# Kernel optimization log

Measured on AMD Instinct MI355X. Metric: run time of the kernel, lower is better.

The kernel has to match this reference:

```python
import jax, jax.numpy as jnp
import numpy as np

D_MODEL = 1024
N_HEADS = 16
D_K = D_MODEL // N_HEADS


def setup_inputs() -> dict:
    key = jax.random.key(0)
    k1, k2, k3, k4, k5 = jax.random.split(key, 5)
    scale = 1.0 / np.sqrt(D_MODEL)
    return {
        "x": jax.random.normal(k1, (4, 2048, D_MODEL), dtype=jnp.float32),
        "w_qkv": jax.random.normal(k2, (D_MODEL, 3 * D_MODEL), dtype=jnp.float32) * scale,
        "b_qkv": jnp.zeros((3 * D_MODEL,), dtype=jnp.float32),
        "w_out": jax.random.normal(k3, (D_MODEL, D_MODEL), dtype=jnp.float32) * scale,
        "b_out": jnp.zeros((D_MODEL,), dtype=jnp.float32),
    }


def reference(x, w_qkv, b_qkv, w_out, b_out):
    B, T, E = x.shape
    qkv = x @ w_qkv + b_qkv                      # [B,T,3E]
    qkv = qkv.reshape(B, T, 3, N_HEADS, D_K)
    qkv = jnp.transpose(qkv, (2, 0, 3, 1, 4))    # [3,B,H,T,d_k]
    q, k, v = qkv[0], qkv[1], qkv[2]
    scores = jnp.einsum("bhqd,bhkd->bhqk", q, k) / jnp.sqrt(jnp.float32(D_K))
    attn = jax.nn.softmax(scores, axis=-1)       # [B,H,T,T]
    out = jnp.einsum("bhqk,bhkd->bhqd", attn, v)  # [B,H,T,d_k]
    out = jnp.transpose(out, (0, 2, 1, 3)).reshape(B, T, E)
    return out @ w_out + b_out
```

## Files before the change

kernel.cpp:

```cpp
#include <hip/hip_runtime.h>
#include <hip/hip_bf16.h>

typedef __attribute__((ext_vector_type(8))) short short8;
typedef __attribute__((ext_vector_type(4))) float f32x4;
typedef __attribute__((ext_vector_type(4))) unsigned short ushort4v;
typedef unsigned short ushort;

#define DEVI static __device__ __forceinline__

DEVI ushort f2bf(float f){
  union { float f; unsigned u; } v; v.f = f;
  unsigned r = v.u + 0x7fffu + ((v.u >> 16) & 1u);
  return (ushort)(r >> 16);
}
DEVI float bf2f(ushort u){
  union { unsigned u; float f; } v; v.u = ((unsigned)u) << 16;
  return v.f;
}

DEVI void gload_lds16(const void* g, void* l){
  __builtin_amdgcn_global_load_lds(
      (const __attribute__((address_space(1))) void*)g,
      (__attribute__((address_space(3))) void*)l, 16, 0, 0);
}

__global__ __launch_bounds__(256) void cast_bf16(const float4* __restrict__ in,
                                                 ushort* __restrict__ out, int n4){
  int i = blockIdx.x * 256 + threadIdx.x;
  if (i < n4){
    float4 v = in[i];
    ushort4v o = { f2bf(v.x), f2bf(v.y), f2bf(v.z), f2bf(v.w) };
    *(ushort4v*)&out[(size_t)i * 4] = o;
  }
}

template<int SPLIT>
__global__ __launch_bounds__(256) void transpose_cast(const float* __restrict__ in,
                                                      ushort* __restrict__ outT,
                                                      ushort* __restrict__ outLo,
                                                      int R, int C){
  __shared__ float tile[64][65];
  const int r0 = blockIdx.y * 64, c0 = blockIdx.x * 64;
  const int t = threadIdx.x;
  for (int it = 0; it < 16; ++it){
    int idx = it * 256 + t; int rr = idx >> 6, cc = idx & 63;
    tile[rr][cc] = in[(size_t)(r0 + rr) * C + (c0 + cc)];
  }
  __syncthreads();
  for (int it = 0; it < 16; ++it){
    int idx = it * 256 + t; int oc = idx >> 6, orow = idx & 63;
    float v = tile[orow][oc];
    ushort hi = f2bf(v);
    size_t o = (size_t)(c0 + oc) * R + (r0 + orow);
    outT[o] = hi;
    if (SPLIT) outLo[o] = f2bf(v - bf2f(hi));
  }
}

__global__ __launch_bounds__(256) void gemm_qk(const ushort* __restrict__ A,
                                               const ushort* __restrict__ BT,
                                               const float* __restrict__ bias,
                                               ushort* __restrict__ Qo,
                                               ushort* __restrict__ Ko){
  constexpr int K = 1024;
  constexpr float QSCALE = 0.18033688011112042f;
  __shared__ __align__(16) ushort As[128 * 32];
  __shared__ __align__(16) ushort Bs[128 * 32];
  const int tid = threadIdx.x, w = tid >> 6, l = tid & 63;
  const int wr = w >> 1, wc = w & 1;
  const int mtile = blockIdx.y * 128, ntile = blockIdx.x * 128;

  f32x4 acc[4][4];
  for (int m = 0; m < 4; ++m) for (int n = 0; n < 4; ++n)
    for (int r = 0; r < 4; ++r) acc[m][n][r] = 0.f;

  const int c0 = 2 * w, c1 = 2 * w + 1;
  const ushort* aG0 = A  + (size_t)(mtile + c0 * 16 + (l >> 2)) * K + (l & 3) * 8;
  const ushort* aG1 = A  + (size_t)(mtile + c1 * 16 + (l >> 2)) * K + (l & 3) * 8;
  const ushort* bG0 = BT + (size_t)(ntile + c0 * 16 + (l >> 2)) * K + (l & 3) * 8;
  const ushort* bG1 = BT + (size_t)(ntile + c1 * 16 + (l >> 2)) * K + (l & 3) * 8;

  for (int kt = 0; kt < K / 32; ++kt){
    __syncthreads();
    gload_lds16(aG0 + kt * 32, &As[c0 * 512]);
    gload_lds16(aG1 + kt * 32, &As[c1 * 512]);
    gload_lds16(bG0 + kt * 32, &Bs[c0 * 512]);
    gload_lds16(bG1 + kt * 32, &Bs[c1 * 512]);
    __syncthreads();
    short8 aF[4], bF[4];
    for (int m = 0; m < 4; ++m)
      aF[m] = *(const short8*)&As[(wr * 64 + m * 16 + (l & 15)) * 32 + (l >> 4) * 8];
    for (int n = 0; n < 4; ++n)
      bF[n] = *(const short8*)&Bs[(wc * 64 + n * 16 + (l & 15)) * 32 + (l >> 4) * 8];
    for (int m = 0; m < 4; ++m)
      for (int n = 0; n < 4; ++n)
        acc[m][n] = __builtin_amdgcn_mfma_f32_16x16x32_bf16(aF[m], bF[n], acc[m][n], 0, 0, 0);
  }

  for (int nf = 0; nf < 4; ++nf){
    int ncol = ntile + wc * 64 + nf * 16 + (l & 15);
    float bv = bias[ncol];
    int isQ = (ncol < 1024) ? 1 : 0;
    int h = (ncol >> 6) & 15, d = ncol & 63;
    ushort* dst = isQ ? Qo : Ko;
    float sc = isQ ? QSCALE : 1.0f;
    for (int m = 0; m < 4; ++m){
      int rbase = mtile + wr * 64 + m * 16 + (l >> 4) * 4;
      for (int r = 0; r < 4; ++r){
        int row = rbase + r;
        int b = row >> 11, t = row & 2047;
        dst[((size_t)(b * 16 + h) * 2048 + t) * 64 + d] = f2bf((acc[m][nf][r] + bv) * sc);
      }
    }
  }
}

__global__ __launch_bounds__(256) void gemm_vT(const ushort* __restrict__ A,
                                               const ushort* __restrict__ BT,
                                               const float* __restrict__ bias,
                                               ushort* __restrict__ VT){
  constexpr int K = 1024;
  __shared__ __align__(16) ushort As[128 * 32];
  __shared__ __align__(16) ushort Bs[128 * 32];
  __shared__ __align__(16) ushort LT[128][136];
  const int tid = threadIdx.x, w = tid >> 6, l = tid & 63;
  const int wr = w >> 1, wc = w & 1;
  const int mtile = blockIdx.y * 128, ntv = blockIdx.x * 128;

  f32x4 acc[4][4];
  for (int m = 0; m < 4; ++m) for (int n = 0; n < 4; ++n)
    for (int r = 0; r < 4; ++r) acc[m][n][r] = 0.f;

  const int c0 = 2 * w, c1 = 2 * w + 1;
  const ushort* aG0 = A  + (size_t)(mtile + c0 * 16 + (l >> 2)) * K + (l & 3) * 8;
  const ushort* aG1 = A  + (size_t)(mtile + c1 * 16 + (l >> 2)) * K + (l & 3) * 8;
  const ushort* bG0 = BT + (size_t)(2048 + ntv + c0 * 16 + (l >> 2)) * K + (l & 3) * 8;
  const ushort* bG1 = BT + (size_t)(2048 + ntv + c1 * 16 + (l >> 2)) * K + (l & 3) * 8;

  for (int kt = 0; kt < K / 32; ++kt){
    __syncthreads();
    gload_lds16(aG0 + kt * 32, &As[c0 * 512]);
    gload_lds16(aG1 + kt * 32, &As[c1 * 512]);
    gload_lds16(bG0 + kt * 32, &Bs[c0 * 512]);
    gload_lds16(bG1 + kt * 32, &Bs[c1 * 512]);
    __syncthreads();
    short8 aF[4], bF[4];
    for (int m = 0; m < 4; ++m)
      aF[m] = *(const short8*)&As[(wr * 64 + m * 16 + (l & 15)) * 32 + (l >> 4) * 8];
    for (int n = 0; n < 4; ++n)
      bF[n] = *(const short8*)&Bs[(wc * 64 + n * 16 + (l & 15)) * 32 + (l >> 4) * 8];
    for (int m = 0; m < 4; ++m)
      for (int n = 0; n < 4; ++n)
        acc[m][n] = __builtin_amdgcn_mfma_f32_16x16x32_bf16(aF[m], bF[n], acc[m][n], 0, 0, 0);
  }

  for (int nf = 0; nf < 4; ++nf){
    int cl = wc * 64 + nf * 16 + (l & 15);
    float bv = bias[2048 + ntv + cl];
    for (int m = 0; m < 4; ++m){
      int rl = wr * 64 + m * 16 + (l >> 4) * 4;
      for (int r = 0; r < 4; ++r)
        LT[cl][rl + r] = f2bf(acc[m][nf][r] + bv);
    }
  }
  __syncthreads();
  const int b = mtile >> 11, t0 = mtile & 2047;
  for (int p = 0; p < 8; ++p){
    int idx = p * 256 + tid;
    int col = idx >> 4, tc = idx & 15;
    int ncol = ntv + col;
    int h = ncol >> 6, d = ncol & 63;
    short8 v = *(const short8*)&LT[col][tc * 8];
    *(short8*)&VT[((size_t)(b * 16 + h) * 64 + d) * 2048 + t0 + tc * 8] = v;
  }
}

__global__ __launch_bounds__(256) void attn_fwd(const ushort* __restrict__ Q,
                                                const ushort* __restrict__ Kb,
                                                const ushort* __restrict__ VT,
                                                ushort* __restrict__ Ohi,
                                                ushort* __restrict__ Olo){
  __shared__ __align__(16) ushort Ks[2][64 * 64];
  __shared__ __align__(16) ushort Vs[2][64 * 64];
  __shared__ __align__(16) ushort Ps[4][16][72];
  const int tid = threadIdx.x, w = tid >> 6, l = tid & 63;
  const int h = l >> 4, q = l & 15;
  const int bh = blockIdx.y, qbase = blockIdx.x * 64;
  const ushort* Qp = Q  + (size_t)bh * 2048 * 64;
  const ushort* Kp = Kb + (size_t)bh * 2048 * 64;
  const ushort* Vp = VT + (size_t)bh * 64 * 2048;

  constexpr float DEFER_THR = 8.0f;

  const int qrow = qbase + w * 16 + q;
  short8 qf0 = *(const short8*)&Qp[(size_t)qrow * 64 + h * 8];
  short8 qf1 = *(const short8*)&Qp[(size_t)qrow * 64 + 32 + h * 8];

  float mrow = -1e30f, lrow = 0.f;
  f32x4 oacc[4];
  for (int c = 0; c < 4; ++c) for (int r = 0; r < 4; ++r) oacc[c][r] = 0.f;

  const int c0 = 2 * w, c1 = 2 * w + 1;
  const int ssrc = ((l & 7) ^ (l >> 3)) * 8;
  const int sr0 = c0 * 8 + (l >> 3), sr1 = c1 * 8 + (l >> 3);
  const int rxor = (q & 7) * 8;

  gload_lds16(Kp + (size_t)sr0 * 64 + ssrc, &Ks[0][c0 * 512]);
  gload_lds16(Kp + (size_t)sr1 * 64 + ssrc, &Ks[0][c1 * 512]);
  gload_lds16(Vp + (size_t)sr0 * 2048 + ssrc, &Vs[0][c0 * 512]);
  gload_lds16(Vp + (size_t)sr1 * 2048 + ssrc, &Vs[0][c1 * 512]);
  __syncthreads();

  int cur = 0;
  for (int kt = 0; kt < 32; ++kt){
    if (kt < 31){
      const int kb = (kt + 1) * 64;
      gload_lds16(Kp + (size_t)(kb + sr0) * 64 + ssrc, &Ks[cur ^ 1][c0 * 512]);
      gload_lds16(Kp + (size_t)(kb + sr1) * 64 + ssrc, &Ks[cur ^ 1][c1 * 512]);
      gload_lds16(Vp + (size_t)sr0 * 2048 + kb + ssrc, &Vs[cur ^ 1][c0 * 512]);
      gload_lds16(Vp + (size_t)sr1 * 2048 + kb + ssrc, &Vs[cur ^ 1][c1 * 512]);
    }
    const ushort* ks = Ks[cur];
    const ushort* vs = Vs[cur];

    f32x4 s[4];
    for (int nf = 0; nf < 4; ++nf) for (int r = 0; r < 4; ++r) s[nf][r] = 0.f;
    __builtin_amdgcn_s_setprio(1);
    for (int nf = 0; nf < 4; ++nf){
      int rb = (nf * 16 + q) * 64;
      short8 kf0 = *(const short8*)&ks[rb + ((h * 8)      ^ rxor)];
      short8 kf1 = *(const short8*)&ks[rb + ((h * 8 + 32) ^ rxor)];
      s[nf] = __builtin_amdgcn_mfma_f32_16x16x32_bf16(kf0, qf0, s[nf], 0, 0, 0);
      s[nf] = __builtin_amdgcn_mfma_f32_16x16x32_bf16(kf1, qf1, s[nf], 0, 0, 0);
    }
    __builtin_amdgcn_s_setprio(0);

    float pm01 = fmaxf(fmaxf(s[0][0], s[0][1]), fmaxf(s[0][2], s[0][3]));
    float pm23 = fmaxf(fmaxf(s[1][0], s[1][1]), fmaxf(s[1][2], s[1][3]));
    float pm45 = fmaxf(fmaxf(s[2][0], s[2][1]), fmaxf(s[2][2], s[2][3]));
    float pm67 = fmaxf(fmaxf(s[3][0], s[3][1]), fmaxf(s[3][2], s[3][3]));
    float pmax = fmaxf(fmaxf(pm01, pm23), fmaxf(pm45, pm67));
    pmax = fmaxf(pmax, __shfl_xor(pmax, 16));
    pmax = fmaxf(pmax, __shfl_xor(pmax, 32));

    if (!__all(pmax <= mrow + DEFER_THR)){
      float mn = fmaxf(mrow, pmax);
      float alpha = __builtin_amdgcn_exp2f(mrow - mn);
      mrow = mn;
      lrow *= alpha;
      for (int c = 0; c < 4; ++c)
        for (int r = 0; r < 4; ++r) oacc[c][r] *= alpha;
    }

    float rsum = 0.f;
    for (int nf = 0; nf < 4; ++nf)
      for (int r = 0; r < 4; ++r){
        float p = __builtin_amdgcn_exp2f(s[nf][r] - mrow);
        s[nf][r] = p; rsum += p;
      }
    rsum += __shfl_xor(rsum, 16);
    rsum += __shfl_xor(rsum, 32);
    lrow += rsum;

    for (int nf = 0; nf < 4; ++nf){
      unsigned pk01, pk23;
      asm("v_cvt_pk_bf16_f32 %0, %1, %2" : "=v"(pk01) : "v"(s[nf][0]), "v"(s[nf][1]));
      asm("v_cvt_pk_bf16_f32 %0, %1, %2" : "=v"(pk23) : "v"(s[nf][2]), "v"(s[nf][3]));
      int key = nf * 16 + 4 * h;
      *(unsigned*)&Ps[w][q][key]     = pk01;
      *(unsigned*)&Ps[w][q][key + 2] = pk23;
    }

    __builtin_amdgcn_s_setprio(1);
    for (int st = 0; st < 2; ++st){
      short8 pf = *(const short8*)&Ps[w][q][st * 32 + h * 8];
      for (int c = 0; c < 4; ++c){
        int vb = (c * 16 + q) * 64;
        short8 vf = *(const short8*)&vs[vb + ((st * 32 + h * 8) ^ rxor)];
        oacc[c] = __builtin_amdgcn_mfma_f32_16x16x32_bf16(vf, pf, oacc[c], 0, 0, 0);
      }
    }
    __builtin_amdgcn_s_setprio(0);

    __syncthreads();
    cur ^= 1;
  }

  const int b = bh >> 4, hh = bh & 15;
  float inv = 1.0f / lrow;
  size_t rowoff = ((size_t)(b * 2048 + qrow)) * 1024 + hh * 64;
  for (int c = 0; c < 4; ++c){
    int d0 = c * 16 + 4 * h;
    for (int pr = 0; pr < 2; ++pr){
      float v0 = oacc[c][2 * pr]     * inv;
      float v1 = oacc[c][2 * pr + 1] * inv;
      ushort h0 = f2bf(v0), h1 = f2bf(v1);
      unsigned hi = (unsigned)h0 | ((unsigned)h1 << 16);
      unsigned lo = (unsigned)f2bf(v0 - bf2f(h0)) | ((unsigned)f2bf(v1 - bf2f(h1)) << 16);
      *(unsigned*)&Ohi[rowoff + d0 + 2 * pr] = hi;
      *(unsigned*)&Olo[rowoff + d0 + 2 * pr] = lo;
    }
  }
}

__global__ __launch_bounds__(256) void gemm_out(const ushort* __restrict__ Ah,
                                                const ushort* __restrict__ Al,
                                                const ushort* __restrict__ BhT,
                                                const ushort* __restrict__ BlT,
                                                const float* __restrict__ bias,
                                                float* __restrict__ out){
  constexpr int K = 1024;
  __shared__ __align__(16) ushort Ash[128 * 32], Asl[128 * 32];
  __shared__ __align__(16) ushort Bsh[128 * 32], Bsl[128 * 32];
  const int tid = threadIdx.x, w = tid >> 6, l = tid & 63;
  const int wr = w >> 1, wc = w & 1;
  const int mtile = blockIdx.y * 128, ntile = blockIdx.x * 128;

  f32x4 acc[4][4];
  for (int m = 0; m < 4; ++m) for (int n = 0; n < 4; ++n)
    for (int r = 0; r < 4; ++r) acc[m][n][r] = 0.f;

  const int c0 = 2 * w, c1 = 2 * w + 1;
  const size_t aOff0 = (size_t)(mtile + c0 * 16 + (l >> 2)) * K + (l & 3) * 8;
  const size_t aOff1 = (size_t)(mtile + c1 * 16 + (l >> 2)) * K + (l & 3) * 8;
  const size_t bOff0 = (size_t)(ntile + c0 * 16 + (l >> 2)) * K + (l & 3) * 8;
  const size_t bOff1 = (size_t)(ntile + c1 * 16 + (l >> 2)) * K + (l & 3) * 8;

  for (int kt = 0; kt < K / 32; ++kt){
    __syncthreads();
    gload_lds16(Ah  + aOff0 + kt * 32, &Ash[c0 * 512]);
    gload_lds16(Ah  + aOff1 + kt * 32, &Ash[c1 * 512]);
    gload_lds16(Al  + aOff0 + kt * 32, &Asl[c0 * 512]);
    gload_lds16(Al  + aOff1 + kt * 32, &Asl[c1 * 512]);
    gload_lds16(BhT + bOff0 + kt * 32, &Bsh[c0 * 512]);
    gload_lds16(BhT + bOff1 + kt * 32, &Bsh[c1 * 512]);
    gload_lds16(BlT + bOff0 + kt * 32, &Bsl[c0 * 512]);
    gload_lds16(BlT + bOff1 + kt * 32, &Bsl[c1 * 512]);
    __syncthreads();
    short8 aH[4], aL[4], bH[4], bL[4];
    for (int m = 0; m < 4; ++m){
      int o = (wr * 64 + m * 16 + (l & 15)) * 32 + (l >> 4) * 8;
      aH[m] = *(const short8*)&Ash[o];
      aL[m] = *(const short8*)&Asl[o];
    }
    for (int n = 0; n < 4; ++n){
      int o = (wc * 64 + n * 16 + (l & 15)) * 32 + (l >> 4) * 8;
      bH[n] = *(const short8*)&Bsh[o];
      bL[n] = *(const short8*)&Bsl[o];
    }
    for (int m = 0; m < 4; ++m)
      for (int n = 0; n < 4; ++n){
        acc[m][n] = __builtin_amdgcn_mfma_f32_16x16x32_bf16(aH[m], bH[n], acc[m][n], 0, 0, 0);
        acc[m][n] = __builtin_amdgcn_mfma_f32_16x16x32_bf16(aH[m], bL[n], acc[m][n], 0, 0, 0);
        acc[m][n] = __builtin_amdgcn_mfma_f32_16x16x32_bf16(aL[m], bH[n], acc[m][n], 0, 0, 0);
      }
  }

  for (int nf = 0; nf < 4; ++nf){
    int ncol = ntile + wc * 64 + nf * 16 + (l & 15);
    float bv = bias[ncol];
    for (int m = 0; m < 4; ++m){
      int rbase = mtile + wr * 64 + m * 16 + (l >> 4) * 4;
      for (int r = 0; r < 4; ++r)
        out[(size_t)(rbase + r) * 1024 + ncol] = acc[m][nf][r] + bv;
    }
  }
}

extern "C" void kernel_launch(void* const* d_in, const int* in_sizes, int n_in,
                              void* d_out, int out_size, void* d_ws, size_t ws_size,
                              hipStream_t stream){
  const float* x     = (const float*)d_in[0];
  const float* w_qkv = (const float*)d_in[1];
  const float* b_qkv = (const float*)d_in[2];
  const float* w_out = (const float*)d_in[3];
  const float* b_out = (const float*)d_in[4];
  float* out = (float*)d_out;
  char* ws = (char*)d_ws;

  size_t off = 0;
  auto alloc = [&](size_t bytes){ size_t o = off; off += (bytes + 255) & ~(size_t)255; return o; };
  const size_t SZ_X   = (size_t)8192 * 1024 * 2;
  const size_t SZ_QKV = (size_t)64 * 2048 * 64 * 2;
  size_t o_xb  = alloc(SZ_X);
  size_t o_wq  = alloc((size_t)3072 * 1024 * 2);
  size_t o_q   = alloc(SZ_QKV);
  size_t o_k   = alloc(SZ_QKV);
  size_t o_v   = alloc(SZ_QKV);
  size_t o_olo = alloc(SZ_X);
  size_t o_wh  = alloc((size_t)1024 * 1024 * 2);
  size_t o_wl  = alloc((size_t)1024 * 1024 * 2);

  ushort* xb  = (ushort*)(ws + o_xb);
  ushort* wqT = (ushort*)(ws + o_wq);
  ushort* Qb  = (ushort*)(ws + o_q);
  ushort* Kb  = (ushort*)(ws + o_k);
  ushort* VTb = (ushort*)(ws + o_v);
  ushort* Ohi = (ushort*)(ws + o_xb);
  ushort* Olo = (ushort*)(ws + o_olo);
  ushort* WhT = (ushort*)(ws + o_wh);
  ushort* WlT = (ushort*)(ws + o_wl);

  cast_bf16<<<8192, 256, 0, stream>>>((const float4*)x, xb, 8192 * 1024 / 4);
  transpose_cast<0><<<dim3(48, 16), 256, 0, stream>>>(w_qkv, wqT, nullptr, 1024, 3072);
  transpose_cast<1><<<dim3(16, 16), 256, 0, stream>>>(w_out, WhT, WlT, 1024, 1024);
  gemm_qk<<<dim3(16, 64), 256, 0, stream>>>(xb, wqT, b_qkv, Qb, Kb);
  gemm_vT<<<dim3(8, 64), 256, 0, stream>>>(xb, wqT, b_qkv, VTb);
  attn_fwd<<<dim3(32, 64), 256, 0, stream>>>(Qb, Kb, VTb, Ohi, Olo);
  gemm_out<<<dim3(8, 64), 256, 0, stream>>>(Ohi, Olo, WhT, WlT, b_out, out);
}
```

Baseline: 368.7 us.

## Use 128-query attention blocks with 8 waves and XCD-aware block remapping

The attention kernel now runs 512 threads per block, covering 128 query rows, so each K/V tile loaded into LDS is shared by twice as many waves. Each wave issues one K and one V async load per tile instead of two. Block IDs are remapped so that blocks landing on the same XCD work on the same batch-head, which should improve L2 reuse of K/V. The row-max reduction is also reordered. The trade-offs are fewer blocks in the grid and higher per-block resource use, which may lower occupancy.

```diff
diff --git a/kernel.cpp b/kernel.cpp
--- a/kernel.cpp
+++ b/kernel.cpp
@@ -175,17 +175,22 @@
   }
 }
 
-__global__ __launch_bounds__(256) void attn_fwd(const ushort* __restrict__ Q,
+__global__ __launch_bounds__(512) void attn_fwd(const ushort* __restrict__ Q,
                                                 const ushort* __restrict__ Kb,
                                                 const ushort* __restrict__ VT,
                                                 ushort* __restrict__ Ohi,
                                                 ushort* __restrict__ Olo){
   __shared__ __align__(16) ushort Ks[2][64 * 64];
   __shared__ __align__(16) ushort Vs[2][64 * 64];
-  __shared__ __align__(16) ushort Ps[4][16][72];
+  __shared__ __align__(16) ushort Ps[8][16][72];
   const int tid = threadIdx.x, w = tid >> 6, l = tid & 63;
   const int h = l >> 4, q = l & 15;
-  const int bh = blockIdx.y, qbase = blockIdx.x * 64;
+
+  const int id = blockIdx.y * 16 + blockIdx.x;
+  const int xcd = id & 7, idx = id >> 3;
+  const int bh = xcd * 8 + (idx >> 4);
+  const int qbase = (idx & 15) * 128;
+
   const ushort* Qp = Q  + (size_t)bh * 2048 * 64;
   const ushort* Kp = Kb + (size_t)bh * 2048 * 64;
   const ushort* Vp = VT + (size_t)bh * 64 * 2048;
@@ -200,25 +205,20 @@
   f32x4 oacc[4];
   for (int c = 0; c < 4; ++c) for (int r = 0; r < 4; ++r) oacc[c][r] = 0.f;
 
-  const int c0 = 2 * w, c1 = 2 * w + 1;
   const int ssrc = ((l & 7) ^ (l >> 3)) * 8;
-  const int sr0 = c0 * 8 + (l >> 3), sr1 = c1 * 8 + (l >> 3);
+  const int srow = w * 8 + (l >> 3);
   const int rxor = (q & 7) * 8;
 
-  gload_lds16(Kp + (size_t)sr0 * 64 + ssrc, &Ks[0][c0 * 512]);
-  gload_lds16(Kp + (size_t)sr1 * 64 + ssrc, &Ks[0][c1 * 512]);
-  gload_lds16(Vp + (size_t)sr0 * 2048 + ssrc, &Vs[0][c0 * 512]);
-  gload_lds16(Vp + (size_t)sr1 * 2048 + ssrc, &Vs[0][c1 * 512]);
+  gload_lds16(Kp + (size_t)srow * 64 + ssrc, &Ks[0][w * 512]);
+  gload_lds16(Vp + (size_t)srow * 2048 + ssrc, &Vs[0][w * 512]);
   __syncthreads();
 
   int cur = 0;
   for (int kt = 0; kt < 32; ++kt){
     if (kt < 31){
       const int kb = (kt + 1) * 64;
-      gload_lds16(Kp + (size_t)(kb + sr0) * 64 + ssrc, &Ks[cur ^ 1][c0 * 512]);
-      gload_lds16(Kp + (size_t)(kb + sr1) * 64 + ssrc, &Ks[cur ^ 1][c1 * 512]);
-      gload_lds16(Vp + (size_t)sr0 * 2048 + kb + ssrc, &Vs[cur ^ 1][c0 * 512]);
-      gload_lds16(Vp + (size_t)sr1 * 2048 + kb + ssrc, &Vs[cur ^ 1][c1 * 512]);
+      gload_lds16(Kp + (size_t)(kb + srow) * 64 + ssrc, &Ks[cur ^ 1][w * 512]);
+      gload_lds16(Vp + (size_t)srow * 2048 + kb + ssrc, &Vs[cur ^ 1][w * 512]);
     }
     const ushort* ks = Ks[cur];
     const ushort* vs = Vs[cur];
@@ -235,11 +235,13 @@
     }
     __builtin_amdgcn_s_setprio(0);
 
-    float pm01 = fmaxf(fmaxf(s[0][0], s[0][1]), fmaxf(s[0][2], s[0][3]));
-    float pm23 = fmaxf(fmaxf(s[1][0], s[1][1]), fmaxf(s[1][2], s[1][3]));
-    float pm45 = fmaxf(fmaxf(s[2][0], s[2][1]), fmaxf(s[2][2], s[2][3]));
-    float pm67 = fmaxf(fmaxf(s[3][0], s[3][1]), fmaxf(s[3][2], s[3][3]));
-    float pmax = fmaxf(fmaxf(pm01, pm23), fmaxf(pm45, pm67));
+    float ma = fmaxf(fmaxf(s[0][0], s[0][1]), s[0][2]);
+    ma = fmaxf(fmaxf(ma, s[0][3]), s[1][0]);
+    ma = fmaxf(fmaxf(ma, s[1][1]), s[1][2]);
+    float mb = fmaxf(fmaxf(s[1][3], s[2][0]), s[2][1]);
+    mb = fmaxf(fmaxf(mb, s[2][2]), s[2][3]);
+    mb = fmaxf(fmaxf(mb, s[3][0]), s[3][1]);
+    float pmax = fmaxf(fmaxf(ma, mb), fmaxf(s[3][2], s[3][3]));
     pmax = fmaxf(pmax, __shfl_xor(pmax, 16));
     pmax = fmaxf(pmax, __shfl_xor(pmax, 32));
 
@@ -406,6 +408,6 @@
   transpose_cast<1><<<dim3(16, 16), 256, 0, stream>>>(w_out, WhT, WlT, 1024, 1024);
   gemm_qk<<<dim3(16, 64), 256, 0, stream>>>(xb, wqT, b_qkv, Qb, Kb);
   gemm_vT<<<dim3(8, 64), 256, 0, stream>>>(xb, wqT, b_qkv, VTb);
-  attn_fwd<<<dim3(32, 64), 256, 0, stream>>>(Qb, Kb, VTb, Ohi, Olo);
+  attn_fwd<<<dim3(16, 64), 512, 0, stream>>>(Qb, Kb, VTb, Ohi, Olo);
   gemm_out<<<dim3(8, 64), 256, 0, stream>>>(Ohi, Olo, WhT, WlT, b_out, out);
 }
```

Result: faster. 339.4 us (-7.9%).
